# Kernel optimization log

Hardware: AMD Instinct MI355X
Metric: run time of the kernel (lower is better)

## Reference

```python
import jax, jax.numpy as jnp
import numpy as np

VOCAB, H, B, L = 32000, 1024, 64, 256  # L leaves per complete binary tree


def setup_inputs() -> dict:
    key = jax.random.key(0)
    ks = jax.random.split(key, 12)
    s = 1.0 / np.sqrt(H)
    return {
        "tokens": jax.random.randint(ks[0], (B, L), 0, VOCAB),
        "emb":    jax.random.normal(ks[1], (VOCAB, H), jnp.float32) * 0.02,
        "W_iock": jax.random.normal(ks[2], (H, 3 * H), jnp.float32) * s,
        "b_iock": jax.random.normal(ks[3], (3 * H,), jnp.float32) * s,
        "U_iock": jax.random.normal(ks[4], (H, 3 * H), jnp.float32) * s,
        "W_fl":   jax.random.normal(ks[5], (H, H), jnp.float32) * s,
        "b_fl":   jax.random.normal(ks[6], (H,), jnp.float32) * s,
        "U_fl":   jax.random.normal(ks[7], (H, H), jnp.float32) * s,
        "W_fr":   jax.random.normal(ks[8], (H, H), jnp.float32) * s,
        "b_fr":   jax.random.normal(ks[9], (H,), jnp.float32) * s,
        "U_fr":   jax.random.normal(ks[10], (H, H), jnp.float32) * s,
    }


def _tree_lstm_levels(h, c, W_iock, b_iock, U_iock, W_fl, b_fl, U_fl, W_fr, b_fr, U_fr):
    """Bottom-up level sweep over a complete binary tree.

    h, c: (B, n, H) states of the current level. Each pass merges sibling
    pairs with the BinaryTreeLSTMCell.calculate gate math.
    """
    outs = []
    while h.shape[1] > 1:
        hl, hr = h[:, 0::2], h[:, 1::2]          # (B, n/2, H)
        cl, cr = c[:, 0::2], c[:, 1::2]
        # iock = W_iock(h_left) + U_iock(h_right); split -> i, o, c~
        iock = hl @ W_iock + hr @ U_iock + b_iock
        i_g, o_g, ck = jnp.split(iock, 3, axis=-1)
        fl = jax.nn.sigmoid(hl @ W_fl + hr @ U_fl + b_fl)
        fr = jax.nn.sigmoid(hl @ W_fr + hr @ U_fr + b_fr)
        c = jax.nn.sigmoid(i_g) * jnp.tanh(ck) + fl * cl + fr * cr
        h = jax.nn.sigmoid(o_g) * jnp.tanh(c)
        outs.append(h)
    forest_output = jnp.concatenate(outs, axis=1)  # (B, L-1, H) internal-node hiddens
    return forest_output, h, c


def reference(tokens, emb, W_iock, b_iock, U_iock, W_fl, b_fl, U_fl, W_fr, b_fr, U_fr):
    h = emb[tokens]                 # leaf hidden = embedding, (B, L, H)
    c = jnp.zeros_like(h)           # leaf memory cell = zeros
    forest_output, h_root, c_root = _tree_lstm_levels(
        h, c, W_iock, b_iock, U_iock, W_fl, b_fl, U_fl, W_fr, b_fr, U_fr)
    # (forest_output, (h, c)) with h, c as (1, B, H) like transpose(0, 1)
    return forest_output, (h_root.transpose(1, 0, 2), c_root.transpose(1, 0, 2))
```

## Files before the change

kernel.cpp:

```cpp
#include <hip/hip_runtime.h>
#include <stdint.h>

#define H     1024
#define K2    2048
#define NTOT  5120
#define BATCH 64
#define BM 128
#define BN 128
#define BK 64

typedef unsigned short u16;
typedef __attribute__((ext_vector_type(8))) short short8;
typedef __attribute__((ext_vector_type(4))) float floatx4;

__device__ __forceinline__ float bf2f(u16 u) {
    return __uint_as_float(((uint32_t)u) << 16);
}
__device__ __forceinline__ u16 f2bf(float f) {
    uint32_t u = __float_as_uint(f);
    u += 0x7fffu + ((u >> 16) & 1u);
    return (u16)(u >> 16);
}
__device__ __forceinline__ uint32_t pk2(float lo, float hi) {
    return (uint32_t)f2bf(lo) | ((uint32_t)f2bf(hi) << 16);
}
__device__ __forceinline__ float sigf(float x) {
    return 1.0f / (1.0f + __expf(-x));
}
__device__ __forceinline__ float tanh_(float x) {
    float e = __expf(-2.0f * fabsf(x));
    float r = (1.0f - e) / (1.0f + e);
    return copysignf(r, x);
}

__global__ void pack_weights(const float* __restrict__ Wio, const float* __restrict__ Uio,
                             const float* __restrict__ Wfl, const float* __restrict__ Ufl,
                             const float* __restrict__ Wfr, const float* __restrict__ Ufr,
                             u16* __restrict__ WT) {
    __shared__ u16 tile[32][33];
    int k0 = blockIdx.x * 32;
    int n0 = blockIdx.y * 32;
    const float *Wp, *Up; int ncols, nloc;
    if (n0 < 3072)      { Wp = Wio; Up = Uio; ncols = 3072; nloc = n0; }
    else if (n0 < 4096) { Wp = Wfl; Up = Ufl; ncols = 1024; nloc = n0 - 3072; }
    else                { Wp = Wfr; Up = Ufr; ncols = 1024; nloc = n0 - 4096; }
    int t = threadIdx.x;
    int c = t & 31, r = t >> 5;
#pragma unroll
    for (int i = 0; i < 4; ++i) {
        int rr = r + i * 8;
        int k = k0 + rr;
        float v = (k < 1024) ? Wp[(long)k * ncols + nloc + c]
                             : Up[(long)(k - 1024) * ncols + nloc + c];
        tile[rr][c] = f2bf(v);
    }
    __syncthreads();
#pragma unroll
    for (int i = 0; i < 4; ++i) {
        int rr = r + i * 8;
        WT[(long)(n0 + rr) * K2 + k0 + c] = tile[c][rr];
    }
}

__global__ void leaf_pack(const int* __restrict__ tokens, const float* __restrict__ emb,
                          u16* __restrict__ leaf) {
    int idx = blockIdx.x * 256 + threadIdx.x;
    int node = idx >> 8;
    int d4 = idx & 255;
    int tok = tokens[node];
    float4 v = ((const float4*)emb)[(long)tok * 256 + d4];
    uint2 o; o.x = pk2(v.x, v.y); o.y = pk2(v.z, v.w);
    ((uint2*)leaf)[(long)node * 256 + d4] = o;
}

__global__ void gemm_bt(const u16* __restrict__ A, const u16* __restrict__ BT,
                        float* __restrict__ G, int mc) {
    __shared__ __align__(16) u16 AsBs[16896];
    u16* As = AsBs;
    u16* Bs = AsBs + 8192;
    float* epi = (float*)AsBs;
    int tid  = threadIdx.x;
    int lane = tid & 63;
    int w    = tid >> 6;
    int wm   = w >> 1, wn = w & 1;
    int rowTile = blockIdx.x * BM;
    int n0      = blockIdx.y * BN;

    const u16* asrc[4];
    const u16* bsrc[4];
#pragma unroll
    for (int cc = 0; cc < 4; ++cc) {
        int r = cc * 32 + w * 8 + (lane >> 3);
        int j = rowTile + r; if (j >= mc) j = mc - 1;
        asrc[cc] = A + (long)j * K2 + (lane & 7) * 8;
        bsrc[cc] = BT + (long)(n0 + r) * K2 + (lane & 7) * 8;
    }

    floatx4 acc[4][4];
#pragma unroll
    for (int mt = 0; mt < 4; ++mt)
#pragma unroll
        for (int nt = 0; nt < 4; ++nt)
            acc[mt][nt] = (floatx4){0.f, 0.f, 0.f, 0.f};

    for (int k0 = 0; k0 < K2; k0 += BK) {
#pragma unroll
        for (int cc = 0; cc < 4; ++cc) {
            __builtin_amdgcn_global_load_lds(
                (const __attribute__((address_space(1))) void*)(asrc[cc] + k0),
                (__attribute__((address_space(3))) void*)(As + cc * 2048 + w * 512), 16, 0, 0);
            __builtin_amdgcn_global_load_lds(
                (const __attribute__((address_space(1))) void*)(bsrc[cc] + k0),
                (__attribute__((address_space(3))) void*)(Bs + cc * 2048 + w * 512), 16, 0, 0);
        }
        __syncthreads();
#pragma unroll
        for (int kb = 0; kb < 2; ++kb) {
            int kfo = kb * 32 + (lane >> 4) * 8;
            short8 af[4], bfv[4];
#pragma unroll
            for (int mt = 0; mt < 4; ++mt)
                af[mt] = *(const short8*)&As[(wm * 64 + mt * 16 + (lane & 15)) * BK + kfo];
#pragma unroll
            for (int nt = 0; nt < 4; ++nt)
                bfv[nt] = *(const short8*)&Bs[(wn * 64 + nt * 16 + (lane & 15)) * BK + kfo];
#pragma unroll
            for (int mt = 0; mt < 4; ++mt)
#pragma unroll
                for (int nt = 0; nt < 4; ++nt)
                    acc[mt][nt] = __builtin_amdgcn_mfma_f32_16x16x32_bf16(
                        af[mt], bfv[nt], acc[mt][nt], 0, 0, 0);
        }
        __syncthreads();
    }

#pragma unroll
    for (int s = 0; s < 2; ++s) {
        if (wm == s) {
#pragma unroll
            for (int mt = 0; mt < 4; ++mt)
#pragma unroll
                for (int r = 0; r < 4; ++r) {
                    int lrow = mt * 16 + (lane >> 4) * 4 + r;
#pragma unroll
                    for (int nt = 0; nt < 4; ++nt)
                        epi[lrow * 132 + wn * 64 + nt * 16 + (lane & 15)] = acc[mt][nt][r];
                }
        }
        __syncthreads();
        int gr0 = rowTile + s * 64;
#pragma unroll
        for (int k = 0; k < 8; ++k) {
            int f4 = tid + k * 256;
            int row = f4 >> 5, c4 = f4 & 31;
            if (gr0 + row < mc) {
                float4 v = *(const float4*)&epi[row * 132 + c4 * 4];
                *(float4*)&G[(long)(gr0 + row) * NTOT + n0 + c4 * 4] = v;
            }
        }
        __syncthreads();
    }
}

#define SWZ2(r) (((r) >> 1) & 3)

template <int BMW>
__global__ __launch_bounds__(512, 2) void gemmF(const u16* __restrict__ A,
                                                const u16* __restrict__ BT,
                                                const float* __restrict__ bio,
                                                const float* __restrict__ bfl,
                                                const float* __restrict__ bfr,
                                                const void* __restrict__ c_in,
                                                void* __restrict__ c_out, int c_bf16,
                                                float* __restrict__ outF,
                                                u16* __restrict__ hnext,
                                                int lp, int level_off, int gm) {
    constexpr int MF    = BMW / 64;
    constexpr int NA    = BMW / 64;
    constexpr int ABASE = (BMW / 128) * 8192;
    constexpr int BUFU  = ABASE + 20480;
    __shared__ __align__(16) u16 lds[2 * BUFU];
    const int tid  = threadIdx.x;
    const int lane = tid & 63;
    const int w    = tid >> 6;
    const int wm   = w >> 1;
    const int wd   = w & 1;

    int f = blockIdx.x;
    int xcd = f & 7, c = f >> 3;
    int by = (xcd & 1) * 8 + (c & 7);
    int bx = (xcd >> 1) * (gm >> 2) + (c >> 3);
    long rowTile = (long)bx * BMW;
    int d0 = by * 64;

    const u16* srcA[NA];
    {
        int rr_ = w * 16 + (lane >> 2);
        int ck_ = ((lane & 3) ^ SWZ2(rr_)) * 8;
#pragma unroll
        for (int cc = 0; cc < NA; ++cc)
            srcA[cc] = A + (rowTile + (cc >> 1) * 128 + rr_) * (long)K2 + (cc & 1) * 32 + ck_;
    }
    const u16* srcB[5];
    {
        int sr_ = (w >> 1) * 16 + (lane >> 2);
        int ck_ = ((lane & 3) ^ SWZ2(sr_)) * 8;
#pragma unroll
        for (int g = 0; g < 5; ++g)
            srcB[g] = BT + (long)(g * 1024 + d0 + sr_) * K2 + (w & 1) * 32 + ck_;
    }

    const int qv = lane >> 4;
    int rA[MF];
#pragma unroll
    for (int mf = 0; mf < MF; ++mf) {
        int rg = wm * (MF * 16) + mf * 16 + (lane & 15);
        int half = rg >> 7, rl = rg & 127;
        rA[mf] = half * 8192 + rl * 32 + ((qv ^ SWZ2(rl)) * 8);
    }
    int rB[2];
#pragma unroll
    for (int sub = 0; sub < 2; ++sub) {
        int rb = wd * 32 + sub * 16 + (lane & 15);
        rB[sub] = rb * 32 + ((qv ^ SWZ2(rb)) * 8);
    }

    floatx4 acc[MF][10];
#pragma unroll
    for (int mf = 0; mf < MF; ++mf)
#pragma unroll
        for (int nf = 0; nf < 10; ++nf)
            acc[mf][nf] = (floatx4){0.f, 0.f, 0.f, 0.f};

#define GF_STAGE(TT, DD)                                                             \
    do {                                                                             \
        _Pragma("unroll")                                                            \
        for (int cc = 0; cc < NA; ++cc)                                              \
            __builtin_amdgcn_global_load_lds(                                        \
                (const __attribute__((address_space(1))) void*)(srcA[cc] + (TT) * 64),\
                (__attribute__((address_space(3))) void*)(lds + (DD) * BUFU + (cc >> 1) * 8192 + (cc & 1) * 4096 + tid * 8), 16, 0, 0); \
        _Pragma("unroll")                                                            \
        for (int g = 0; g < 5; ++g)                                                  \
            __builtin_amdgcn_global_load_lds(                                        \
                (const __attribute__((address_space(1))) void*)(srcB[g] + (TT) * 64),\
                (__attribute__((address_space(3))) void*)(lds + (DD) * BUFU + ABASE + g * 4096 + (w & 1) * 2048 + (w >> 1) * 512 + lane * 8), 16, 0, 0); \
    } while (0)

    GF_STAGE(0, 0);

    for (int t = 0; t < 32; ++t) {
        int d = t & 1;
        asm volatile("s_barrier" ::: "memory");
        if (t < 31) {
            GF_STAGE(t + 1, d ^ 1);
            asm volatile("s_waitcnt vmcnt(%0)" :: "i"(NA + 5) : "memory");
        } else {
            asm volatile("s_waitcnt vmcnt(0)" ::: "memory");
        }
        asm volatile("s_barrier" ::: "memory");
        const u16* bufD = lds + d * BUFU;
#pragma unroll
        for (int ks = 0; ks < 2; ++ks) {
            short8 aF[MF];
#pragma unroll
            for (int mf = 0; mf < MF; ++mf)
                aF[mf] = *(const short8*)&bufD[rA[mf] + ks * 4096];
#pragma unroll
            for (int g = 0; g < 5; ++g) {
                short8 bF[2];
#pragma unroll
                for (int sub = 0; sub < 2; ++sub)
                    bF[sub] = *(const short8*)&bufD[ABASE + g * 4096 + ks * 2048 + rB[sub]];
                __builtin_amdgcn_s_setprio(1);
#pragma unroll
                for (int mf = 0; mf < MF; ++mf)
#pragma unroll
                    for (int sub = 0; sub < 2; ++sub)
                        acc[mf][g * 2 + sub] = __builtin_amdgcn_mfma_f32_16x16x32_bf16(
                            aF[mf], bF[sub], acc[mf][g * 2 + sub], 0, 0, 0);
                __builtin_amdgcn_s_setprio(0);
            }
        }
    }
#undef GF_STAGE

    float bI[2], bO[2], bC[2], bL[2], bR[2];
    int dsub[2];
#pragma unroll
    for (int sub = 0; sub < 2; ++sub) {
        int dd = d0 + wd * 32 + sub * 16 + (lane & 15);
        dsub[sub] = dd;
        bI[sub] = bio[dd]; bO[sub] = bio[1024 + dd]; bC[sub] = bio[2048 + dd];
        bL[sub] = bfl[dd]; bR[sub] = bfr[dd];
    }
    int pmask = (1 << lp) - 1;
    int has_c = (c_in != nullptr);
#pragma unroll
    for (int mf = 0; mf < MF; ++mf) {
#pragma unroll
        for (int rr = 0; rr < 4; ++rr) {
            int row = wm * (MF * 16) + mf * 16 + (lane >> 4) * 4 + rr;
            long J = rowTile + row;
            int b = (int)(J >> lp), p = (int)(J & pmask);
            long ho = ((long)b * 255 + level_off + p) * H;
#pragma unroll
            for (int sub = 0; sub < 2; ++sub) {
                int dd = dsub[sub];
                float i_  = acc[mf][0 + sub][rr] + bI[sub];
                float o_  = acc[mf][2 + sub][rr] + bO[sub];
                float ck_ = acc[mf][4 + sub][rr] + bC[sub];
                float cv = sigf(i_) * tanh_(ck_);
                if (has_c) {
                    float fl_ = sigf(acc[mf][6 + sub][rr] + bL[sub]);
                    float fr_ = sigf(acc[mf][8 + sub][rr] + bR[sub]);
                    float cl, cr;
                    if (c_bf16) {
                        cl = bf2f(__builtin_nontemporal_load(
                                 (const u16*)c_in + (2 * J) * H + dd));
                        cr = bf2f(__builtin_nontemporal_load(
                                 (const u16*)c_in + (2 * J + 1) * H + dd));
                    } else {
                        cl = __builtin_nontemporal_load(
                                 (const float*)c_in + (2 * J) * H + dd);
                        cr = __builtin_nontemporal_load(
                                 (const float*)c_in + (2 * J + 1) * H + dd);
                    }
                    cv += fl_ * cl + fr_ * cr;
                }
                float hv = sigf(o_) * tanh_(cv);
                __builtin_nontemporal_store(hv, &outF[ho + dd]);
                if (c_bf16)
                    __builtin_nontemporal_store(f2bf(cv), (u16*)c_out + J * H + dd);
                else
                    __builtin_nontemporal_store(cv, (float*)c_out + J * H + dd);
                __builtin_nontemporal_store(f2bf(hv), hnext + J * H + dd);
            }
        }
    }
}

__global__ __launch_bounds__(512, 2) void gemmS(const u16* __restrict__ A,
                                                const u16* __restrict__ BT,
                                                float* __restrict__ P,
                                                int RT, int KS, int NT,
                                                int mLim, int mPad) {
    constexpr int ABASE = 8192;
    constexpr int BUFU  = 28672;
    __shared__ __align__(16) u16 lds[2 * BUFU];
    const int tid  = threadIdx.x;
    const int lane = tid & 63;
    const int w    = tid >> 6;
    const int wm   = w >> 1;
    const int wd   = w & 1;

    int nwg = RT * 16 * KS;
    int f = blockIdx.x;
    int q = nwg >> 3, r = nwg & 7;
    int xcd = f & 7, rank = f >> 3;
    int wg = (xcd < r ? xcd * (q + 1) : r * (q + 1) + (xcd - r) * q) + rank;
    int bx  = wg % RT;
    int by  = (wg / RT) % 16;
    int ksx = wg / (RT * 16);
    long rowTile = (long)bx * 128;
    int d0 = by * 64;
    int kOff = ksx * (NT * 64);

    const u16* srcA[2];
    {
        int rr_ = w * 16 + (lane >> 2);
        int ck_ = ((lane & 3) ^ SWZ2(rr_)) * 8;
#pragma unroll
        for (int c = 0; c < 2; ++c)
            srcA[c] = A + (rowTile + rr_) * (long)K2 + kOff + c * 32 + ck_;
    }
    const u16* srcB[5];
    {
        int sr_ = (w >> 1) * 16 + (lane >> 2);
        int ck_ = ((lane & 3) ^ SWZ2(sr_)) * 8;
#pragma unroll
        for (int g = 0; g < 5; ++g)
            srcB[g] = BT + (long)(g * 1024 + d0 + sr_) * K2 + kOff + (w & 1) * 32 + ck_;
    }

    const int qv = lane >> 4;
    int rA[2];
#pragma unroll
    for (int mf = 0; mf < 2; ++mf) {
        int rl = wm * 32 + mf * 16 + (lane & 15);
        rA[mf] = rl * 32 + ((qv ^ SWZ2(rl)) * 8);
    }
    int rB[2];
#pragma unroll
    for (int sub = 0; sub < 2; ++sub) {
        int rb = wd * 32 + sub * 16 + (lane & 15);
        rB[sub] = rb * 32 + ((qv ^ SWZ2(rb)) * 8);
    }

    floatx4 acc[2][10];
#pragma unroll
    for (int mf = 0; mf < 2; ++mf)
#pragma unroll
        for (int nf = 0; nf < 10; ++nf)
            acc[mf][nf] = (floatx4){0.f, 0.f, 0.f, 0.f};

#define GS_STAGE(TT, DD)                                                             \
    do {                                                                             \
        _Pragma("unroll")                                                            \
        for (int c = 0; c < 2; ++c)                                                  \
            __builtin_amdgcn_global_load_lds(                                        \
                (const __attribute__((address_space(1))) void*)(srcA[c] + (TT) * 64),\
                (__attribute__((address_space(3))) void*)(lds + (DD) * BUFU + c * 4096 + tid * 8), 16, 0, 0); \
        _Pragma("unroll")                                                            \
        for (int g = 0; g < 5; ++g)                                                  \
            __builtin_amdgcn_global_load_lds(                                        \
                (const __attribute__((address_space(1))) void*)(srcB[g] + (TT) * 64),\
                (__attribute__((address_space(3))) void*)(lds + (DD) * BUFU + ABASE + g * 4096 + (w & 1) * 2048 + (w >> 1) * 512 + lane * 8), 16, 0, 0); \
    } while (0)

    GS_STAGE(0, 0);

    for (int t = 0; t < NT; ++t) {
        int d = t & 1;
        asm volatile("s_barrier" ::: "memory");
        if (t < NT - 1) {
            GS_STAGE(t + 1, d ^ 1);
            asm volatile("s_waitcnt vmcnt(7)" ::: "memory");
        } else {
            asm volatile("s_waitcnt vmcnt(0)" ::: "memory");
        }
        asm volatile("s_barrier" ::: "memory");
        const u16* bufD = lds + d * BUFU;
#pragma unroll
        for (int ks = 0; ks < 2; ++ks) {
            short8 aF[2];
#pragma unroll
            for (int mf = 0; mf < 2; ++mf)
                aF[mf] = *(const short8*)&bufD[rA[mf] + ks * 4096];
#pragma unroll
            for (int g = 0; g < 5; ++g) {
                short8 bF[2];
#pragma unroll
                for (int sub = 0; sub < 2; ++sub)
                    bF[sub] = *(const short8*)&bufD[ABASE + g * 4096 + ks * 2048 + rB[sub]];
                __builtin_amdgcn_s_setprio(1);
#pragma unroll
                for (int mf = 0; mf < 2; ++mf)
#pragma unroll
                    for (int sub = 0; sub < 2; ++sub)
                        acc[mf][g * 2 + sub] = __builtin_amdgcn_mfma_f32_16x16x32_bf16(
                            aF[mf], bF[sub], acc[mf][g * 2 + sub], 0, 0, 0);
                __builtin_amdgcn_s_setprio(0);
            }
        }
    }
#undef GS_STAGE

    int dsub[2];
#pragma unroll
    for (int sub = 0; sub < 2; ++sub)
        dsub[sub] = d0 + wd * 32 + sub * 16 + (lane & 15);
#pragma unroll
    for (int mf = 0; mf < 2; ++mf) {
#pragma unroll
        for (int rr = 0; rr < 4; ++rr) {
            int row = wm * 32 + mf * 16 + (lane >> 4) * 4 + rr;
            long J = rowTile + row;
            if (J < mLim) {
                long pb = ((long)ksx * mPad + J) * NTOT;
#pragma unroll
                for (int g = 0; g < 5; ++g)
#pragma unroll
                    for (int sub = 0; sub < 2; ++sub)
                        P[pb + g * 1024 + dsub[sub]] = acc[mf][g * 2 + sub][rr];
            }
        }
    }
}

__global__ void redgate(const float* __restrict__ P, const float* __restrict__ bio,
                        const float* __restrict__ bfl, const float* __restrict__ bfr,
                        const void* __restrict__ c_in, void* __restrict__ c_out, int c_bf16,
                        float* __restrict__ outF, u16* __restrict__ hnext,
                        int lp, int level_off, int mc, int KS, int mPad) {
    int idx = blockIdx.x * 256 + threadIdx.x;
    int j = idx >> 8;
    if (j >= mc) return;
    int d = (idx & 255) * 4;
    int b = j >> lp, p = j & ((1 << lp) - 1);
    float ac[5][4] = {};
    for (int s = 0; s < KS; ++s) {
        long pb = ((long)s * mPad + j) * NTOT + d;
#pragma unroll
        for (int g = 0; g < 5; ++g) {
            float4 v = *(const float4*)&P[pb + g * 1024];
            ac[g][0] += v.x; ac[g][1] += v.y; ac[g][2] += v.z; ac[g][3] += v.w;
        }
    }
    float4 bi = *(const float4*)&bio[d];
    float4 bo = *(const float4*)&bio[1024 + d];
    float4 bc = *(const float4*)&bio[2048 + d];
    float4 bl = *(const float4*)&bfl[d];
    float4 br = *(const float4*)&bfr[d];
    const float* fbi = (const float*)&bi; const float* fbo = (const float*)&bo;
    const float* fbc = (const float*)&bc; const float* fbl = (const float*)&bl;
    const float* fbr = (const float*)&br;
    float clv[4], crv[4];
    {
        long cb = ((long)b * (2 << lp) + 2 * p) * H + d;
        if (c_bf16) {
            uint2 ul = *(const uint2*)((const u16*)c_in + cb);
            uint2 ur = *(const uint2*)((const u16*)c_in + cb + H);
            clv[0] = bf2f((u16)ul.x); clv[1] = bf2f((u16)(ul.x >> 16));
            clv[2] = bf2f((u16)ul.y); clv[3] = bf2f((u16)(ul.y >> 16));
            crv[0] = bf2f((u16)ur.x); crv[1] = bf2f((u16)(ur.x >> 16));
            crv[2] = bf2f((u16)ur.y); crv[3] = bf2f((u16)(ur.y >> 16));
        } else {
            float4 l4 = *(const float4*)((const float*)c_in + cb);
            float4 r4 = *(const float4*)((const float*)c_in + cb + H);
            clv[0] = l4.x; clv[1] = l4.y; clv[2] = l4.z; clv[3] = l4.w;
            crv[0] = r4.x; crv[1] = r4.y; crv[2] = r4.z; crv[3] = r4.w;
        }
    }
    float cv[4], hv[4];
#pragma unroll
    for (int qq = 0; qq < 4; ++qq) {
        float c = sigf(ac[0][qq] + fbi[qq]) * tanh_(ac[2][qq] + fbc[qq]);
        c += sigf(ac[3][qq] + fbl[qq]) * clv[qq] + sigf(ac[4][qq] + fbr[qq]) * crv[qq];
        cv[qq] = c;
        hv[qq] = sigf(ac[1][qq] + fbo[qq]) * tanh_(c);
    }
    long co = (long)j * H + d;
    if (c_bf16) {
        uint2 oc; oc.x = pk2(cv[0], cv[1]); oc.y = pk2(cv[2], cv[3]);
        *(uint2*)((u16*)c_out + co) = oc;
    } else {
        *(float4*)((float*)c_out + co) = make_float4(cv[0], cv[1], cv[2], cv[3]);
    }
    long oi = ((long)b * 255 + level_off + p) * H + d;
    *(float4*)&outF[oi] = make_float4(hv[0], hv[1], hv[2], hv[3]);
    uint2 oh; oh.x = pk2(hv[0], hv[1]); oh.y = pk2(hv[2], hv[3]);
    *(uint2*)(hnext + (long)j * H + d) = oh;
}

__global__ void gates(const float* __restrict__ G, const float* __restrict__ bio,
                      const float* __restrict__ bfl, const float* __restrict__ bfr,
                      const void* __restrict__ c_in, void* __restrict__ c_out, int c_bf16,
                      float* __restrict__ outF, u16* __restrict__ hnext,
                      int lp, int level_off, int row0, int mc) {
    int idx = blockIdx.x * 256 + threadIdx.x;
    int j = idx >> 8;
    if (j >= mc) return;
    int d = (idx & 255) * 4;
    int J = row0 + j;
    int b = J >> lp, p = J & ((1 << lp) - 1);
    long gb = (long)j * NTOT;
    float4 gi = *(const float4*)&G[gb + d];
    float4 go = *(const float4*)&G[gb + 1024 + d];
    float4 gc = *(const float4*)&G[gb + 2048 + d];
    float4 gl = *(const float4*)&G[gb + 3072 + d];
    float4 gr = *(const float4*)&G[gb + 4096 + d];
    float4 bi = *(const float4*)&bio[d];
    float4 bo = *(const float4*)&bio[1024 + d];
    float4 bc = *(const float4*)&bio[2048 + d];
    float4 bl = *(const float4*)&bfl[d];
    float4 br = *(const float4*)&bfr[d];
    float clv[4] = {0.f, 0.f, 0.f, 0.f}, crv[4] = {0.f, 0.f, 0.f, 0.f};
    if (c_in) {
        long cb = ((long)b * (2 << lp) + 2 * p) * H + d;
        if (c_bf16) {
            uint2 ul = *(const uint2*)((const u16*)c_in + cb);
            uint2 ur = *(const uint2*)((const u16*)c_in + cb + H);
            clv[0] = bf2f((u16)ul.x); clv[1] = bf2f((u16)(ul.x >> 16));
            clv[2] = bf2f((u16)ul.y); clv[3] = bf2f((u16)(ul.y >> 16));
            crv[0] = bf2f((u16)ur.x); crv[1] = bf2f((u16)(ur.x >> 16));
            crv[2] = bf2f((u16)ur.y); crv[3] = bf2f((u16)(ur.y >> 16));
        } else {
            float4 l4 = *(const float4*)((const float*)c_in + cb);
            float4 r4 = *(const float4*)((const float*)c_in + cb + H);
            clv[0] = l4.x; clv[1] = l4.y; clv[2] = l4.z; clv[3] = l4.w;
            crv[0] = r4.x; crv[1] = r4.y; crv[2] = r4.z; crv[3] = r4.w;
        }
    }
    const float* fgi = (const float*)&gi; const float* fgo = (const float*)&go;
    const float* fgc = (const float*)&gc; const float* fgl = (const float*)&gl;
    const float* fgr = (const float*)&gr;
    const float* fbi = (const float*)&bi; const float* fbo = (const float*)&bo;
    const float* fbc = (const float*)&bc; const float* fbl = (const float*)&bl;
    const float* fbr = (const float*)&br;
    float cv[4], hv[4];
    int has_c = (c_in != nullptr);
#pragma unroll
    for (int qq = 0; qq < 4; ++qq) {
        float c = sigf(fgi[qq] + fbi[qq]) * tanh_(fgc[qq] + fbc[qq]);
        if (has_c)
            c += sigf(fgl[qq] + fbl[qq]) * clv[qq] + sigf(fgr[qq] + fbr[qq]) * crv[qq];
        cv[qq] = c;
        hv[qq] = sigf(fgo[qq] + fbo[qq]) * tanh_(c);
    }
    long co = (long)J * H + d;
    if (c_bf16) {
        uint2 oc; oc.x = pk2(cv[0], cv[1]); oc.y = pk2(cv[2], cv[3]);
        *(uint2*)((u16*)c_out + co) = oc;
    } else {
        *(float4*)((float*)c_out + co) = make_float4(cv[0], cv[1], cv[2], cv[3]);
    }
    long oi = ((long)b * 255 + level_off + p) * H + d;
    *(float4*)&outF[oi] = make_float4(hv[0], hv[1], hv[2], hv[3]);
    uint2 oh; oh.x = pk2(hv[0], hv[1]); oh.y = pk2(hv[2], hv[3]);
    *(uint2*)(hnext + (long)J * H + d) = oh;
}

__global__ void root_copy(const float* __restrict__ outF, const void* __restrict__ c_root,
                          int c_bf16, float* __restrict__ tail) {
    int idx = blockIdx.x * 256 + threadIdx.x;
    if (idx < 65536) {
        int b = idx >> 10, d = idx & 1023;
        tail[idx] = outF[((long)b * 255 + 254) * H + d];
    } else {
        int i2 = idx - 65536;
        tail[idx] = c_bf16 ? bf2f(((const u16*)c_root)[i2]) : ((const float*)c_root)[i2];
    }
}

extern "C" void kernel_launch(void* const* d_in, const int* in_sizes, int n_in,
                              void* d_out, int out_size, void* d_ws, size_t ws_size,
                              hipStream_t stream) {
    const int* tokens = (const int*)d_in[0];
    const float* emb = (const float*)d_in[1];
    const float* Wio = (const float*)d_in[2];
    const float* bio = (const float*)d_in[3];
    const float* Uio = (const float*)d_in[4];
    const float* Wfl = (const float*)d_in[5];
    const float* bfl = (const float*)d_in[6];
    const float* Ufl = (const float*)d_in[7];
    const float* Wfr = (const float*)d_in[8];
    const float* bfr = (const float*)d_in[9];
    const float* Ufr = (const float*)d_in[10];
    float* outF = (float*)d_out;

    char* ws = (char*)d_ws;
    size_t off = 0;
    u16* WT   = (u16*)(ws + off); off += (size_t)NTOT * K2 * 2;
    u16* leaf = (u16*)(ws + off); off += (size_t)BATCH * 256 * H * 2;
    u16* hE   = (u16*)(ws + off); off += (size_t)8192 * H * 2;
    u16* hO   = (u16*)(ws + off); off += (size_t)4096 * H * 2;
    size_t cEf = (size_t)8192 * H, cOf = (size_t)4096 * H;
    int c_bf16 = (ws_size >= off + (cEf + cOf) * 4 + (size_t)512 * NTOT * 4) ? 0 : 1;
    size_t csz = c_bf16 ? 2 : 4;
    void* cE = (void*)(ws + off); off += cEf * csz;
    void* cO = (void*)(ws + off); off += cOf * csz;
    size_t avail = (ws_size > off) ? (ws_size - off) : 0;
    size_t Pbytes = (size_t)2048 * NTOT * 4;
    int splitOK = (avail >= Pbytes);
    float* P = (float*)(ws + off);
    long Grows = (long)(avail / ((size_t)NTOT * 4));
    if (Grows > 512) Grows = 512;
    Grows &= ~127L;
    if (Grows < 128) Grows = 128;
    float* G = (float*)(ws + off);

    pack_weights<<<dim3(64, 160), 256, 0, stream>>>(Wio, Uio, Wfl, Ufl, Wfr, Ufr, WT);
    leaf_pack<<<16384, 256, 0, stream>>>(tokens, emb, leaf);

    const int off_out[8] = {0, 128, 192, 224, 240, 248, 252, 254};
    for (int li = 0; li < 8; ++li) {
        int lp = 7 - li;
        long m = (long)BATCH << lp;
        const u16* Acur = (li == 0) ? leaf : ((li & 1) ? hE : hO);
        u16* hnext = (li & 1) ? hO : hE;
        const void* c_in = (li == 0) ? nullptr : ((li & 1) ? cE : cO);
        void* c_out = (li & 1) ? cO : cE;
        if (m >= 4096) {
            int gm = (int)(m >> 8);
            gemmF<256><<<gm * 16, 512, 0, stream>>>(Acur, WT, bio, bfl, bfr,
                                                    c_in, c_out, c_bf16, outF, hnext,
                                                    lp, off_out[li], gm);
        } else if (m >= 2048) {
            int gm = (int)(m >> 7);
            gemmF<128><<<gm * 16, 512, 0, stream>>>(Acur, WT, bio, bfl, bfr,
                                                    c_in, c_out, c_bf16, outF, hnext,
                                                    lp, off_out[li], gm);
        } else if (splitOK) {
            int KS = (m == 1024) ? 2 : (m == 512) ? 4 : (m == 256) ? 8 : 16;
            int RT = (m >= 128) ? (int)(m >> 7) : 1;
            int mPad = RT * 128;
            int NT = 32 / KS;
            gemmS<<<RT * 16 * KS, 512, 0, stream>>>(Acur, WT, P, RT, KS, NT,
                                                    (int)m, mPad);
            redgate<<<(int)m, 256, 0, stream>>>(P, bio, bfl, bfr, c_in, c_out, c_bf16,
                                                outF, hnext, lp, off_out[li],
                                                (int)m, KS, mPad);
        } else {
            for (long row0 = 0; row0 < m; row0 += Grows) {
                int mc = (int)((m - row0 > Grows) ? Grows : (m - row0));
                dim3 grid((mc + BM - 1) / BM, NTOT / BN);
                gemm_bt<<<grid, 256, 0, stream>>>(Acur + row0 * K2, WT, G, mc);
                gates<<<mc, 256, 0, stream>>>(G, bio, bfl, bfr, c_in, c_out, c_bf16,
                                              outF, hnext, lp, off_out[li], (int)row0, mc);
            }
        }
    }
    root_copy<<<512, 256, 0, stream>>>(outF, cO, c_bf16, outF + (size_t)BATCH * 255 * H);
}
```

Baseline: 706.0 us.

## Interleave per-group B-tile prefetch with MFMA groups in the fused gate GEMM

The K loop previously issued all of the next stage's A and B global-to-LDS loads up front, then waited and ran a barrier before any compute. Now the next stage's A tile is issued first, and the five B column-group loads are spread between the per-group MFMA batches. Each batch is preceded by a fine-grained vmcnt wait and a barrier, so compute on early groups overlaps the remaining loads. Fragments for both k-substeps are held in registers at once. This adds several barriers per iteration and makes correctness depend on hand-tuned vmcnt counts, in exchange for less exposed load latency.

```diff
diff --git a/kernel.cpp b/kernel.cpp
--- a/kernel.cpp
+++ b/kernel.cpp
@@ -177,6 +177,7 @@
                                                 int lp, int level_off, int gm) {
     constexpr int MF    = BMW / 64;
     constexpr int NA    = BMW / 64;
+    constexpr int TOT   = NA + 5;
     constexpr int ABASE = (BMW / 128) * 8192;
     constexpr int BUFU  = ABASE + 20480;
     __shared__ __align__(16) u16 lds[2 * BUFU];
@@ -232,57 +233,74 @@
         for (int nf = 0; nf < 10; ++nf)
             acc[mf][nf] = (floatx4){0.f, 0.f, 0.f, 0.f};
 
-#define GF_STAGE(TT, DD)                                                             \
+#define GF_STAGE_A(TT, DD)                                                           \
     do {                                                                             \
         _Pragma("unroll")                                                            \
         for (int cc = 0; cc < NA; ++cc)                                              \
             __builtin_amdgcn_global_load_lds(                                        \
                 (const __attribute__((address_space(1))) void*)(srcA[cc] + (TT) * 64),\
                 (__attribute__((address_space(3))) void*)(lds + (DD) * BUFU + (cc >> 1) * 8192 + (cc & 1) * 4096 + tid * 8), 16, 0, 0); \
+    } while (0)
+
+#define GF_STAGE_B(TT, DD, GG)                                                       \
+    __builtin_amdgcn_global_load_lds(                                                \
+        (const __attribute__((address_space(1))) void*)(srcB[GG] + (TT) * 64),       \
+        (__attribute__((address_space(3))) void*)(lds + (DD) * BUFU + ABASE + (GG) * 4096 + (w & 1) * 2048 + (w >> 1) * 512 + lane * 8), 16, 0, 0)
+
+#define GF_MFMA_G(GG)                                                                \
+    do {                                                                             \
+        __builtin_amdgcn_s_setprio(1);                                               \
         _Pragma("unroll")                                                            \
-        for (int g = 0; g < 5; ++g)                                                  \
-            __builtin_amdgcn_global_load_lds(                                        \
-                (const __attribute__((address_space(1))) void*)(srcB[g] + (TT) * 64),\
-                (__attribute__((address_space(3))) void*)(lds + (DD) * BUFU + ABASE + g * 4096 + (w & 1) * 2048 + (w >> 1) * 512 + lane * 8), 16, 0, 0); \
+        for (int ks = 0; ks < 2; ++ks)                                               \
+            _Pragma("unroll")                                                        \
+            for (int mf = 0; mf < MF; ++mf)                                          \
+                _Pragma("unroll")                                                    \
+                for (int sub = 0; sub < 2; ++sub)                                    \
+                    acc[mf][(GG) * 2 + sub] = __builtin_amdgcn_mfma_f32_16x16x32_bf16( \
+                        aF[ks][mf], bF[ks][sub], acc[mf][(GG) * 2 + sub], 0, 0, 0);  \
+        __builtin_amdgcn_s_setprio(0);                                               \
     } while (0)
 
-    GF_STAGE(0, 0);
-
+    GF_STAGE_A(0, 0);
+#pragma unroll
+    for (int g = 0; g < 5; ++g) GF_STAGE_B(0, 0, g);
+
+    short8 aF[2][MF], bF[2][2];
     for (int t = 0; t < 32; ++t) {
         int d = t & 1;
+        const u16* bufD = lds + d * BUFU;
+        bool last = (t == 31);
+        asm volatile("s_waitcnt vmcnt(%0)" :: "i"(TOT - NA - 1) : "memory");
         asm volatile("s_barrier" ::: "memory");
-        if (t < 31) {
-            GF_STAGE(t + 1, d ^ 1);
-            asm volatile("s_waitcnt vmcnt(%0)" :: "i"(NA + 5) : "memory");
-        } else {
-            asm volatile("s_waitcnt vmcnt(0)" ::: "memory");
-        }
-        asm volatile("s_barrier" ::: "memory");
-        const u16* bufD = lds + d * BUFU;
 #pragma unroll
         for (int ks = 0; ks < 2; ++ks) {
-            short8 aF[MF];
 #pragma unroll
             for (int mf = 0; mf < MF; ++mf)
-                aF[mf] = *(const short8*)&bufD[rA[mf] + ks * 4096];
-#pragma unroll
-            for (int g = 0; g < 5; ++g) {
-                short8 bF[2];
+                aF[ks][mf] = *(const short8*)&bufD[rA[mf] + ks * 4096];
+#pragma unroll
+            for (int sub = 0; sub < 2; ++sub)
+                bF[ks][sub] = *(const short8*)&bufD[ABASE + ks * 2048 + rB[sub]];
+        }
+        if (!last) GF_STAGE_A(t + 1, d ^ 1);
+        GF_MFMA_G(0);
+#pragma unroll
+        for (int g = 1; g < 5; ++g) {
+            if (!last) asm volatile("s_waitcnt vmcnt(%0)" :: "i"(TOT - 2) : "memory");
+            else       asm volatile("s_waitcnt vmcnt(%0)" :: "i"(4 - g) : "memory");
+            asm volatile("s_barrier" ::: "memory");
+#pragma unroll
+            for (int ks = 0; ks < 2; ++ks)
 #pragma unroll
                 for (int sub = 0; sub < 2; ++sub)
-                    bF[sub] = *(const short8*)&bufD[ABASE + g * 4096 + ks * 2048 + rB[sub]];
-                __builtin_amdgcn_s_setprio(1);
-#pragma unroll
-                for (int mf = 0; mf < MF; ++mf)
-#pragma unroll
-                    for (int sub = 0; sub < 2; ++sub)
-                        acc[mf][g * 2 + sub] = __builtin_amdgcn_mfma_f32_16x16x32_bf16(
-                            aF[mf], bF[sub], acc[mf][g * 2 + sub], 0, 0, 0);
-                __builtin_amdgcn_s_setprio(0);
-            }
-        }
-    }
-#undef GF_STAGE
+                    bF[ks][sub] = *(const short8*)&bufD[ABASE + g * 4096 + ks * 2048 + rB[sub]];
+            if (!last) GF_STAGE_B(t + 1, d ^ 1, g - 1);
+            GF_MFMA_G(g);
+        }
+        if (!last) GF_STAGE_B(t + 1, d ^ 1, 4);
+    }
+#undef GF_STAGE_A
+#undef GF_STAGE_B
+#undef GF_MFMA_G
 
     float bI[2], bO[2], bC[2], bL[2], bR[2];
     int dsub[2];
```

New measurement: 661.3 us. 6.3% less time.
